# Optimization experiments

Hardware: AMD Instinct MI355X
Metric: run time of the kernel (lower is better)

The kernel has to match this reference:

```python
import jax, jax.numpy as jnp
import numpy as np

DELTA = 16
KAPPA = 4
ACTION_LOSS_WEIGHT = 0.2
ACTION_CLASS_WEIGHT = 10.0
NEG = -1e30  # sentinel for masked-out positions

B, T = 1024, 4096


def setup_inputs() -> dict:
    key = jax.random.key(0)
    k1, k2, k3, k4 = jax.random.split(key, 4)
    s1s2_log_probs = jax.random.normal(k1, (B, T, 2), dtype=jnp.float32)
    action_log_probs = jax.random.normal(k2, (B, T, 1), dtype=jnp.float32)
    lens = jax.random.randint(k3, (B,), T // 2, T + 1, dtype=jnp.int32)
    video_level_scores = jax.random.uniform(k4, (B,), dtype=jnp.float32)
    return {
        "s1s2_log_probs": s1s2_log_probs,
        "action_log_probs": action_log_probs,
        "lens": lens,
        "video_level_scores": video_level_scores,
    }


def _optimal_state_change(s1s2_probs, action_probs, lens):
    """Per-video optimal (state1, action, state2) alignment with delta spacing.

    Maximizes p1[s1] * pa[ac] * p2[s2] s.t. s1 <= ac - DELTA, ac + DELTA <= s2 < len,
    via prefix/suffix cumulative maxima (O(T) DP per video, fully vectorized).
    Returns integer targets: state_targets in {0,1,2}, action_targets in {0,1,2}.
    """
    Bn, Tn, _ = s1s2_probs.shape
    p1, p2 = s1s2_probs[..., 0], s1s2_probs[..., 1]
    pa = action_probs[..., 0]
    t = jnp.arange(Tn)
    valid = t[None, :] < lens[:, None]  # [B,T]
    p1m = jnp.where(valid, p1, NEG)
    p2m = jnp.where(valid, p2, NEG)
    pre = jax.lax.cummax(p1m, axis=1)                                  # max p1[0..t]
    suf = jnp.flip(jax.lax.cummax(jnp.flip(p2m, 1), axis=1), 1)        # max p2[t..T-1]
    pad = jnp.full((Bn, DELTA), NEG, dtype=p1.dtype)
    pre_s = jnp.concatenate([pad, pre[:, : Tn - DELTA]], axis=1)       # best s1 <= ac-DELTA
    suf_s = jnp.concatenate([suf[:, DELTA:], pad], axis=1)             # best s2 >= ac+DELTA
    ok = (pre_s > NEG / 2) & (suf_s > NEG / 2) & valid
    score = jnp.where(ok, pre_s * pa * suf_s, NEG)
    ac = jnp.argmax(score, axis=1)                                     # [B]
    s1 = jnp.argmax(jnp.where(t[None, :] <= (ac - DELTA)[:, None], p1m, NEG), axis=1)
    s2 = jnp.argmax(jnp.where(t[None, :] >= (ac + DELTA)[:, None], p2m, NEG), axis=1)
    state_t = ((t[None, :] == s1[:, None]).astype(jnp.int32)
               + 2 * (t[None, :] == s2[:, None]).astype(jnp.int32))
    dist = jnp.abs(t[None, :] - ac[:, None])
    action_t = jnp.where(valid, jnp.where(dist <= KAPPA, 2, 1), 0)
    return state_t, action_t


def reference(s1s2_log_probs, action_log_probs, lens, video_level_scores):
    s1s2_probs = jax.nn.softmax(s1s2_log_probs, axis=-1)
    action_probs = jax.nn.sigmoid(action_log_probs)
    state_t, action_t = _optimal_state_change(
        jax.lax.stop_gradient(s1s2_probs), jax.lax.stop_gradient(action_probs), lens)

    # state loss: CE over 2 classes, masked where target == 0 (ignore)
    logp = jax.nn.log_softmax(s1s2_log_probs, axis=-1)          # [B,T,2]
    cls = jnp.clip(state_t - 1, 0, None)
    state_loss = -jnp.take_along_axis(logp, cls[..., None], axis=-1)[..., 0]
    state_loss = state_loss * (state_t != 0).astype(logp.dtype)

    # action loss: weighted BCE-with-logits
    z = action_log_probs[..., 0]                                 # [B,T]
    y = (action_t == 2).astype(z.dtype)
    bce = jnp.maximum(z, 0.0) - z * y + jnp.log1p(jnp.exp(-jnp.abs(z)))
    w = (action_t == 1).astype(z.dtype) + ACTION_CLASS_WEIGHT * (action_t == 2).astype(z.dtype)
    action_loss = bce * w

    state_loss = state_loss * video_level_scores[:, None]
    action_loss = action_loss * video_level_scores[:, None]
    return jnp.sum(state_loss), ACTION_LOSS_WEIGHT * jnp.sum(action_loss)
```

## Files before the change

kernel.cpp:

```cpp
#include <hip/hip_runtime.h>
#include <math.h>


#define T_LEN 4096
#define NTH   1024
#define NW    16
#define CH    4
#define PADS  5
#define DCH   4
#define DELTA 16
#define NEGV  (-1e30f)
#define NEGH  (-5e29f)

__device__ __forceinline__ float frcp(float x) { return __builtin_amdgcn_rcpf(x); }

__device__ __forceinline__ void amax_comb(float& v, int& i, float ov, int oi) {
  if (ov > v || (ov == v && oi < i)) { v = ov; i = oi; }
}

__global__ __launch_bounds__(NTH, 8) void lftc_main(
    const float* __restrict__ s1s2,
    const float* __restrict__ act,
    const int*   __restrict__ lens,
    const float* __restrict__ vls,
    float* __restrict__ ws)
{
  __shared__ float P1s[NTH * PADS];
  __shared__ float cm1[NTH];
  __shared__ float cm2[NTH];
  __shared__ float wag1[NW], wag2[NW];
  __shared__ float redv[NW];  __shared__ int redi[NW];
  __shared__ float redv2[NW]; __shared__ int redi2[NW];
  __shared__ float redv3[NW]; __shared__ int redi3[NW];

  const int b    = blockIdx.x;
  const int tid  = threadIdx.x;
  const int lane = tid & 63;
  const int wv   = tid >> 6;
  const int len  = lens[b];

  const float* __restrict__ srow = s1s2 + (size_t)b * T_LEN * 2;
  const float* __restrict__ zrow = act  + (size_t)b * T_LEN;

  const int j    = tid;
  const int base = j * CH;

  float4 sv0, sv1, zv;
  {
    const float4* sp4 = reinterpret_cast<const float4*>(srow + 2 * base);
    sv0 = sp4[0]; sv1 = sp4[1];
    zv  = *reinterpret_cast<const float4*>(zrow + base);
  }
  float z[CH]   = {zv.x, zv.y, zv.z, zv.w};
  float lx[CH]  = {sv0.x, sv0.z, sv1.x, sv1.z};
  float ly[CH]  = {sv0.y, sv0.w, sv1.y, sv1.w};

  float p1r[CH];
  float m1 = NEGV, m2 = NEGV;
#pragma unroll
  for (int i = 0; i < CH; i++) {
    float p   = frcp(1.f + __expf(ly[i] - lx[i]));
    bool  v   = (base + i) < len;
    float p1m = v ? p : NEGV;
    float p2m = v ? 1.f - p : NEGV;
    p1r[i] = p1m;
    P1s[j * PADS + i] = p1m;
    m1 = fmaxf(m1, p1m);
    m2 = fmaxf(m2, p2m);
  }

  {
    float pm = m1;
#pragma unroll
    for (int off = 1; off < 64; off <<= 1) {
      float o = __shfl_up(pm, off);
      if (lane >= off) pm = fmaxf(pm, o);
    }
    float sm = m2;
#pragma unroll
    for (int off = 1; off < 64; off <<= 1) {
      float o = __shfl_down(sm, off);
      if (lane + off < 64) sm = fmaxf(sm, o);
    }
    if (lane == 63) wag1[wv] = pm;
    if (lane == 0)  wag2[wv] = sm;
    __syncthreads();
    float addp = NEGV, adds = NEGV;
#pragma unroll
    for (int q = 0; q < NW; q++) {
      if (q < wv) addp = fmaxf(addp, wag1[q]);
      if (q > wv) adds = fmaxf(adds, wag2[q]);
    }
    cm1[tid] = fmaxf(pm, addp);
    cm2[tid] = fmaxf(sm, adds);
    __syncthreads();
  }

  float best = NEGV;
  int   bidx = base;
  {
    float rs[CH];
    if (j <= NTH - 1 - DCH) {
      float run = (j + DCH + 1 <= NTH - 1) ? cm2[j + DCH + 1] : NEGV;
      const int b2 = (j + DCH) * PADS;
#pragma unroll
      for (int i = CH - 1; i >= 0; --i) {
        float p1n = P1s[b2 + i];
        float p2n = (p1n > NEGH) ? 1.f - p1n : NEGV;
        run = fmaxf(run, p2n);
        rs[i] = run;
      }
    }
    float prerun = (j >= DCH + 1) ? cm1[j - DCH - 1] : NEGV;
    const int b1 = (j - DCH) * PADS;
#pragma unroll
    for (int i = 0; i < CH; i++) {
      float pre_s = NEGV;
      if (j >= DCH) { prerun = fmaxf(prerun, P1s[b1 + i]); pre_s = prerun; }
      float suf_s = (j <= NTH - 1 - DCH) ? rs[i] : NEGV;
      int t = base + i;
      if (pre_s > NEGH && suf_s > NEGH && t < len) {
        float pa = frcp(1.f + __expf(-z[i]));
        float sc = (pre_s * pa) * suf_s;
        if (sc > best) { best = sc; bidx = t; }
      }
    }
  }
#pragma unroll
  for (int off = 32; off; off >>= 1) {
    float ov = __shfl_down(best, off);
    int   oi = __shfl_down(bidx, off);
    amax_comb(best, bidx, ov, oi);
  }
  if (lane == 0) { redv[wv] = best; redi[wv] = bidx; }
  __syncthreads();
  int ac;
  {
    float v = redv[0]; int i = redi[0];
#pragma unroll
    for (int q = 1; q < NW; q++) amax_comb(v, i, redv[q], redi[q]);
    ac = i;
  }

  {
    float v1 = NEGV; int i1 = 0;
    float v2 = NEGV; int i2 = 0;
    const int e1   = ac - DELTA;
    const int s2lo = ac + DELTA;
#pragma unroll
    for (int k = 0; k < CH; k++) {
      int t = base + k;
      float p1v = p1r[k];
      if (t <= e1 && p1v > v1) { v1 = p1v; i1 = t; }
      float p2v = (p1v > NEGH) ? 1.f - p1v : NEGV;
      if (t >= s2lo && p2v > v2) { v2 = p2v; i2 = t; }
    }
#pragma unroll
    for (int off = 32; off; off >>= 1) {
      float ov1 = __shfl_down(v1, off); int oi1 = __shfl_down(i1, off);
      amax_comb(v1, i1, ov1, oi1);
      float ov2 = __shfl_down(v2, off); int oi2 = __shfl_down(i2, off);
      amax_comb(v2, i2, ov2, oi2);
    }
    if (lane == 0) { redv2[wv] = v1; redi2[wv] = i1; redv3[wv] = v2; redi3[wv] = i2; }
  }

  float sp_part = 0.f;
#pragma unroll
  for (int k = 0; k < CH; k++) {
    int t = base + k;
    if (t < len) {
      float zi = z[k];
      float b0 = fmaxf(zi, 0.f) + __logf(1.f + __expf(-fabsf(zi)));
      int d = t - ac;
      sp_part += (d >= -4 && d <= 4) ? 10.f * (b0 - zi) : b0;
    }
  }
  float s = sp_part;
#pragma unroll
  for (int off = 32; off; off >>= 1) s += __shfl_down(s, off);
  if (lane == 0) wag1[wv] = s;
  __syncthreads();
  if (tid == 0) {
    float tot = 0.f;
#pragma unroll
    for (int q = 0; q < NW; q++) tot += wag1[q];

    float sv_1 = redv2[0]; int s1 = redi2[0];
    float sv_2 = redv3[0]; int s2 = redi3[0];
    for (int q = 1; q < NW; q++) {
      amax_comb(sv_1, s1, redv2[q], redi2[q]);
      amax_comb(sv_2, s2, redv3[q], redi3[q]);
    }
    float2 q1 = *reinterpret_cast<const float2*>(srow + 2 * (size_t)s1);
    float2 q2 = *reinterpret_cast<const float2*>(srow + 2 * (size_t)s2);
    float d1 = q1.y - q1.x;
    float loss1 = fmaxf(d1, 0.f) + __logf(1.f + __expf(-fabsf(d1)));
    float d2 = q2.x - q2.y;
    float loss2 = fmaxf(d2, 0.f) + __logf(1.f + __expf(-fabsf(d2)));

    float w = vls[b];
    ws[2 * (size_t)b]     = w * (loss1 + loss2);
    ws[2 * (size_t)b + 1] = 0.2f * w * tot;
  }
}

__global__ void lftc_reduce(const float* __restrict__ ws, float* __restrict__ out, int B) {
  __shared__ float a0[4], a1[4];
  const int tid  = threadIdx.x;
  const int lane = tid & 63;
  const int wv   = tid >> 6;
  float s0 = 0.f, s1 = 0.f;
  const float2* w2 = reinterpret_cast<const float2*>(ws);
  for (int i = tid; i < B; i += 256) {
    float2 p = w2[i];
    s0 += p.x;
    s1 += p.y;
  }
#pragma unroll
  for (int off = 32; off; off >>= 1) {
    s0 += __shfl_down(s0, off);
    s1 += __shfl_down(s1, off);
  }
  if (lane == 0) { a0[wv] = s0; a1[wv] = s1; }
  __syncthreads();
  if (tid == 0) {
    out[0] = a0[0] + a0[1] + a0[2] + a0[3];
    out[1] = a1[0] + a1[1] + a1[2] + a1[3];
  }
}

extern "C" void kernel_launch(void* const* d_in, const int* in_sizes, int n_in,
                              void* d_out, int out_size, void* d_ws, size_t ws_size,
                              hipStream_t stream) {
  const float* s1s2 = (const float*)d_in[0];
  const float* act  = (const float*)d_in[1];
  const int*   lens = (const int*)d_in[2];
  const float* vls  = (const float*)d_in[3];
  float* out = (float*)d_out;
  float* ws  = (float*)d_ws;

  const int B = in_sizes[2];

  lftc_main<<<B, NTH, 0, stream>>>(s1s2, act, lens, vls, ws);
  lftc_reduce<<<1, 256, 0, stream>>>(ws, out, B);
}
```

Measured before the change: 108.6 us.

## Halve block size with 8 elements per thread and fold cross-wave scan into consumers

Drops the block to 512 threads, each handling 8 timesteps with wider vector loads. The cross-wave prefix/suffix combination is no longer a separate pass with an extra barrier; each consumer folds the per-wave aggregates into its boundary value directly. The final state-loss terms are computed by the threads that own s1 and s2 from values already in registers, which removes the serial re-read of global memory by thread 0, and the per-video outputs become a 4-wide workspace slot. The trade-off is higher register pressure per thread and a lower occupancy hint.

```diff
diff --git a/kernel.cpp b/kernel.cpp
--- a/kernel.cpp
+++ b/kernel.cpp
@@ -3,11 +3,11 @@
 
 
 #define T_LEN 4096
-#define NTH   1024
-#define NW    16
-#define CH    4
-#define PADS  5
-#define DCH   4
+#define NTH   512
+#define NW    8
+#define CH    8
+#define PADS  9
+#define DCH   2
 #define DELTA 16
 #define NEGV  (-1e30f)
 #define NEGH  (-5e29f)
@@ -18,7 +18,7 @@
   if (ov > v || (ov == v && oi < i)) { v = ov; i = oi; }
 }
 
-__global__ __launch_bounds__(NTH, 8) void lftc_main(
+__global__ __launch_bounds__(NTH, 6) void lftc_main(
     const float* __restrict__ s1s2,
     const float* __restrict__ act,
     const int*   __restrict__ lens,
@@ -26,18 +26,20 @@
     float* __restrict__ ws)
 {
   __shared__ float P1s[NTH * PADS];
-  __shared__ float cm1[NTH];
-  __shared__ float cm2[NTH];
+  __shared__ float cr1[NTH];
+  __shared__ float cr2[NTH];
   __shared__ float wag1[NW], wag2[NW];
   __shared__ float redv[NW];  __shared__ int redi[NW];
   __shared__ float redv2[NW]; __shared__ int redi2[NW];
   __shared__ float redv3[NW]; __shared__ int redi3[NW];
+  __shared__ float wact[NW];
 
   const int b    = blockIdx.x;
   const int tid  = threadIdx.x;
   const int lane = tid & 63;
   const int wv   = tid >> 6;
   const int len  = lens[b];
+  const float w  = vls[b];
 
   const float* __restrict__ srow = s1s2 + (size_t)b * T_LEN * 2;
   const float* __restrict__ zrow = act  + (size_t)b * T_LEN;
@@ -45,25 +47,24 @@
   const int j    = tid;
   const int base = j * CH;
 
-  float4 sv0, sv1, zv;
+  float4 sv0, sv1, sv2, sv3, zva, zvb;
   {
     const float4* sp4 = reinterpret_cast<const float4*>(srow + 2 * base);
-    sv0 = sp4[0]; sv1 = sp4[1];
-    zv  = *reinterpret_cast<const float4*>(zrow + base);
-  }
-  float z[CH]   = {zv.x, zv.y, zv.z, zv.w};
-  float lx[CH]  = {sv0.x, sv0.z, sv1.x, sv1.z};
-  float ly[CH]  = {sv0.y, sv0.w, sv1.y, sv1.w};
-
-  float p1r[CH];
+    sv0 = sp4[0]; sv1 = sp4[1]; sv2 = sp4[2]; sv3 = sp4[3];
+    const float4* zp4 = reinterpret_cast<const float4*>(zrow + base);
+    zva = zp4[0]; zvb = zp4[1];
+  }
+  float z[CH]  = {zva.x, zva.y, zva.z, zva.w, zvb.x, zvb.y, zvb.z, zvb.w};
+  float dr[CH] = {sv0.y - sv0.x, sv0.w - sv0.z, sv1.y - sv1.x, sv1.w - sv1.z,
+                  sv2.y - sv2.x, sv2.w - sv2.z, sv3.y - sv3.x, sv3.w - sv3.z};
+
   float m1 = NEGV, m2 = NEGV;
 #pragma unroll
   for (int i = 0; i < CH; i++) {
-    float p   = frcp(1.f + __expf(ly[i] - lx[i]));
+    float p   = frcp(1.f + __expf(dr[i]));
     bool  v   = (base + i) < len;
     float p1m = v ? p : NEGV;
     float p2m = v ? 1.f - p : NEGV;
-    p1r[i] = p1m;
     P1s[j * PADS + i] = p1m;
     m1 = fmaxf(m1, p1m);
     m2 = fmaxf(m2, p2m);
@@ -82,26 +83,26 @@
       float o = __shfl_down(sm, off);
       if (lane + off < 64) sm = fmaxf(sm, o);
     }
+    cr1[tid] = pm;
+    cr2[tid] = sm;
     if (lane == 63) wag1[wv] = pm;
     if (lane == 0)  wag2[wv] = sm;
-    __syncthreads();
-    float addp = NEGV, adds = NEGV;
-#pragma unroll
-    for (int q = 0; q < NW; q++) {
-      if (q < wv) addp = fmaxf(addp, wag1[q]);
-      if (q > wv) adds = fmaxf(adds, wag2[q]);
-    }
-    cm1[tid] = fmaxf(pm, addp);
-    cm2[tid] = fmaxf(sm, adds);
-    __syncthreads();
-  }
+  }
+  __syncthreads();
 
   float best = NEGV;
   int   bidx = base;
   {
     float rs[CH];
     if (j <= NTH - 1 - DCH) {
-      float run = (j + DCH + 1 <= NTH - 1) ? cm2[j + DCH + 1] : NEGV;
+      float run = NEGV;
+      if (j + DCH + 1 <= NTH - 1) {
+        int q = j + DCH + 1;
+        run = cr2[q];
+        int wq = q >> 6;
+#pragma unroll
+        for (int u = 1; u < NW; u++) if (u > wq) run = fmaxf(run, wag2[u]);
+      }
       const int b2 = (j + DCH) * PADS;
 #pragma unroll
       for (int i = CH - 1; i >= 0; --i) {
@@ -111,7 +112,14 @@
         rs[i] = run;
       }
     }
-    float prerun = (j >= DCH + 1) ? cm1[j - DCH - 1] : NEGV;
+    float prerun = NEGV;
+    if (j >= DCH + 1) {
+      int q = j - DCH - 1;
+      prerun = cr1[q];
+      int wq = q >> 6;
+#pragma unroll
+      for (int u = 0; u < NW - 1; u++) if (u < wq) prerun = fmaxf(prerun, wag1[u]);
+    }
     const int b1 = (j - DCH) * PADS;
 #pragma unroll
     for (int i = 0; i < CH; i++) {
@@ -147,10 +155,11 @@
     float v2 = NEGV; int i2 = 0;
     const int e1   = ac - DELTA;
     const int s2lo = ac + DELTA;
+    const int bj   = j * PADS;
 #pragma unroll
     for (int k = 0; k < CH; k++) {
       int t = base + k;
-      float p1v = p1r[k];
+      float p1v = P1s[bj + k];
       if (t <= e1 && p1v > v1) { v1 = p1v; i1 = t; }
       float p2v = (p1v > NEGH) ? 1.f - p1v : NEGV;
       if (t >= s2lo && p2v > v2) { v2 = p2v; i2 = t; }
@@ -176,32 +185,35 @@
       sp_part += (d >= -4 && d <= 4) ? 10.f * (b0 - zi) : b0;
     }
   }
-  float s = sp_part;
-#pragma unroll
-  for (int off = 32; off; off >>= 1) s += __shfl_down(s, off);
-  if (lane == 0) wag1[wv] = s;
-  __syncthreads();
-  if (tid == 0) {
-    float tot = 0.f;
-#pragma unroll
-    for (int q = 0; q < NW; q++) tot += wag1[q];
-
+#pragma unroll
+  for (int off = 32; off; off >>= 1) sp_part += __shfl_down(sp_part, off);
+  if (lane == 0) wact[wv] = sp_part;
+  __syncthreads();
+
+  {
     float sv_1 = redv2[0]; int s1 = redi2[0];
     float sv_2 = redv3[0]; int s2 = redi3[0];
+#pragma unroll
     for (int q = 1; q < NW; q++) {
       amax_comb(sv_1, s1, redv2[q], redi2[q]);
       amax_comb(sv_2, s2, redv3[q], redi3[q]);
     }
-    float2 q1 = *reinterpret_cast<const float2*>(srow + 2 * (size_t)s1);
-    float2 q2 = *reinterpret_cast<const float2*>(srow + 2 * (size_t)s2);
-    float d1 = q1.y - q1.x;
-    float loss1 = fmaxf(d1, 0.f) + __logf(1.f + __expf(-fabsf(d1)));
-    float d2 = q2.x - q2.y;
-    float loss2 = fmaxf(d2, 0.f) + __logf(1.f + __expf(-fabsf(d2)));
-
-    float w = vls[b];
-    ws[2 * (size_t)b]     = w * (loss1 + loss2);
-    ws[2 * (size_t)b + 1] = 0.2f * w * tot;
+    if (j == (s1 >> 3)) {
+      float d1 = dr[s1 & 7];
+      float loss1 = fmaxf(d1, 0.f) + __logf(1.f + __expf(-fabsf(d1)));
+      ws[4 * (size_t)b + 0] = w * loss1;
+    }
+    if (j == (s2 >> 3)) {
+      float d2 = -dr[s2 & 7];
+      float loss2 = fmaxf(d2, 0.f) + __logf(1.f + __expf(-fabsf(d2)));
+      ws[4 * (size_t)b + 1] = w * loss2;
+    }
+    if (tid == 0) {
+      float tot = 0.f;
+#pragma unroll
+      for (int q = 0; q < NW; q++) tot += wact[q];
+      ws[4 * (size_t)b + 2] = 0.2f * w * tot;
+    }
   }
 }
 
@@ -211,11 +223,11 @@
   const int lane = tid & 63;
   const int wv   = tid >> 6;
   float s0 = 0.f, s1 = 0.f;
-  const float2* w2 = reinterpret_cast<const float2*>(ws);
+  const float4* w4 = reinterpret_cast<const float4*>(ws);
   for (int i = tid; i < B; i += 256) {
-    float2 p = w2[i];
-    s0 += p.x;
-    s1 += p.y;
+    float4 p = w4[i];
+    s0 += p.x + p.y;
+    s1 += p.z;
   }
 #pragma unroll
   for (int off = 32; off; off >>= 1) {
```

After: 98.87 us. 9.0% less time.
